# Kernel tuning notes

Hardware: AMD Instinct MI355X
Metric: run time of the kernel (lower is better)

## Reference

```python
import jax, jax.numpy as jnp
import numpy as np

B, K, H = 8, 64, 2048
NH, NKV, HD = 16, 4, 128
CTX = 4096
EPS = 1e-6


def _rope_tables(batch, total_len, head_dim):
    inv_freq = 1.0 / (10000.0 ** (np.arange(0, head_dim, 2, dtype=np.float32) / head_dim))
    pos = np.arange(total_len, dtype=np.float32)
    freqs = np.outer(pos, inv_freq)                      # [S, D/2]
    emb = np.concatenate([freqs, freqs], axis=-1)        # [S, D]
    cos = np.broadcast_to(np.cos(emb), (batch, total_len, head_dim))
    sin = np.broadcast_to(np.sin(emb), (batch, total_len, head_dim))
    return jnp.asarray(cos), jnp.asarray(sin)


def setup_inputs() -> dict:
    key = jax.random.key(0)
    ks = jax.random.split(key, 10)
    s = 0.02
    cos, sin = _rope_tables(B, CTX + K, HD)
    return {
        "hidden_states": jax.random.normal(ks[0], (B, K, H), jnp.float32),
        "ctx_k": jax.random.normal(ks[1], (B, CTX, NKV, HD), jnp.float32),
        "ctx_v": jax.random.normal(ks[2], (B, CTX, NKV, HD), jnp.float32),
        "attn_mask": jnp.zeros((B, 1, K, CTX + K), jnp.float32),
        "cos": cos,
        "sin": sin,
        "wq": jax.random.normal(ks[3], (NH * HD, H), jnp.float32) * s,
        "wk": jax.random.normal(ks[4], (NKV * HD, H), jnp.float32) * s,
        "wv": jax.random.normal(ks[5], (NKV * HD, H), jnp.float32) * s,
        "wo": jax.random.normal(ks[6], (H, NH * HD), jnp.float32) * s,
        "q_norm_w": jnp.ones((HD,), jnp.float32),
        "k_norm_w": jnp.ones((HD,), jnp.float32),
    }


def _rms_norm(x, w):
    var = jnp.mean(jnp.square(x), axis=-1, keepdims=True)
    return x * jax.lax.rsqrt(var + EPS) * w


def _rotate_half(x):
    x1, x2 = jnp.split(x, 2, axis=-1)
    return jnp.concatenate([-x2, x1], axis=-1)


def reference(hidden_states, ctx_k, ctx_v, attn_mask, cos, sin,
              wq, wk, wv, wo, q_norm_w, k_norm_w):
    b, k_len, _ = hidden_states.shape
    ctx_len = ctx_k.shape[1]
    groups = NH // NKV

    # projections -> [B, heads, S, D]
    q = (hidden_states @ wq.T).reshape(b, k_len, NH, HD).transpose(0, 2, 1, 3)
    k_noise = (hidden_states @ wk.T).reshape(b, k_len, NKV, HD).transpose(0, 2, 1, 3)
    v_noise = (hidden_states @ wv.T).reshape(b, k_len, NKV, HD).transpose(0, 2, 1, 3)

    # concat context KV (already per-head projected) with noise KV
    k = jnp.concatenate([ctx_k.transpose(0, 2, 1, 3), k_noise], axis=2)  # [B,NKV,ctx+K,D]
    v = jnp.concatenate([ctx_v.transpose(0, 2, 1, 3), v_noise], axis=2)

    # QK RMSNorm over head_dim
    q = _rms_norm(q, q_norm_w)
    k = _rms_norm(k, k_norm_w)

    # RoPE: q occupies the last K positions, k spans all ctx+K positions
    cos_q = cos[:, ctx_len:, :][:, None, :, :]
    sin_q = sin[:, ctx_len:, :][:, None, :, :]
    cos_k = cos[:, None, :, :]
    sin_k = sin[:, None, :, :]
    q = q * cos_q + _rotate_half(q) * sin_q
    k = k * cos_k + _rotate_half(k) * sin_k

    # GQA expand kv heads -> NH heads
    k = jnp.repeat(k, groups, axis=1)  # [B,NH,ctx+K,D]
    v = jnp.repeat(v, groups, axis=1)

    # scaled dot product attention with float mask
    scale = 1.0 / jnp.sqrt(jnp.float32(HD))
    scores = jnp.einsum("bhqd,bhkd->bhqk", q, k) * scale + attn_mask
    probs = jax.nn.softmax(scores, axis=-1)
    attn = jnp.einsum("bhqk,bhkd->bhqd", probs, v)

    out = attn.transpose(0, 2, 1, 3).reshape(b, k_len, NH * HD)
    return out @ wo.T
```

## Files before the change

kernel.cpp:

```cpp
#include <hip/hip_runtime.h>

#define BB   8
#define KQ   64
#define HDIM 2048
#define NH   16
#define NKV  4
#define HD   128
#define CTX  4096
#define TTOT 4160
#define NTILES 65
#define LOG2E 1.4426950408889634f
#define SCALE 0.08838834764831845f
#define QSCALE (SCALE * LOG2E)
#define MFIX 16.34f

typedef unsigned short u16;
typedef unsigned int   u32;
typedef __attribute__((ext_vector_type(8))) short  s16x8;
typedef __attribute__((ext_vector_type(4))) unsigned short u16x4;
typedef __attribute__((ext_vector_type(4))) float  f32x4;
typedef __bf16 bf16x8 __attribute__((ext_vector_type(8)));

__device__ __forceinline__ u16 f2bf(float f) {
    union { __bf16 h; u16 u; } v; v.h = (__bf16)f; return v.u;
}
__device__ __forceinline__ float bf2f(u16 u) {
    union { float f; u32 u; } v; v.u = ((u32)u) << 16;
    return v.f;
}
__device__ __forceinline__ u32 pack2(float a, float b) {
    return (u32)f2bf(a) | ((u32)f2bf(b) << 16);
}
__device__ __forceinline__ f32x4 mfma16(bf16x8 a, bf16x8 b, f32x4 c) {
    return __builtin_amdgcn_mfma_f32_16x16x32_bf16(a, b, c, 0, 0, 0);
}

__global__ __launch_bounds__(256) void cast_all(
    const float* __restrict__ wq, const float* __restrict__ wk,
    const float* __restrict__ wv, const float* __restrict__ wo,
    const float* __restrict__ hs,
    u16* __restrict__ wqkvb, u16* __restrict__ wob, u16* __restrict__ hsb)
{
    const int i = blockIdx.x * 256 + threadIdx.x;
    const float* src; u16* dst;
    if (i < 524288)       { src = wq + (size_t)i * 8;             dst = wqkvb + (size_t)i * 8; }
    else if (i < 655360)  { src = wk + (size_t)(i - 524288) * 8;  dst = wqkvb + (size_t)i * 8; }
    else if (i < 786432)  { src = wv + (size_t)(i - 655360) * 8;  dst = wqkvb + (size_t)i * 8; }
    else if (i < 1310720) { src = wo + (size_t)(i - 786432) * 8;  dst = wob + (size_t)(i - 786432) * 8; }
    else                  { src = hs + (size_t)(i - 1310720) * 8; dst = hsb + (size_t)(i - 1310720) * 8; }
    float4 a = *(const float4*)src;
    float4 b = *(const float4*)(src + 4);
    s16x8 v;
    v[0]=(short)f2bf(a.x); v[1]=(short)f2bf(a.y); v[2]=(short)f2bf(a.z); v[3]=(short)f2bf(a.w);
    v[4]=(short)f2bf(b.x); v[5]=(short)f2bf(b.y); v[6]=(short)f2bf(b.z); v[7]=(short)f2bf(b.w);
    *(s16x8*)dst = v;
}

__global__ __launch_bounds__(256) void prep_mask(
    const float* __restrict__ mask, u16* __restrict__ maskT)
{
    __shared__ float T[64 * 65];
    const int pt = blockIdx.x % 65, b = blockIdx.x / 65;
    const int p0 = pt * 64;
    {
        const int q = threadIdx.x >> 2, pg = (threadIdx.x & 3) * 16;
        const float* src = mask + ((size_t)b * 64 + q) * TTOT + p0 + pg;
#pragma unroll
        for (int v4 = 0; v4 < 4; ++v4) {
            float4 v = *(const float4*)(src + v4 * 4);
            T[q * 65 + pg + v4 * 4 + 0] = fmaf(v.x, LOG2E, -MFIX);
            T[q * 65 + pg + v4 * 4 + 1] = fmaf(v.y, LOG2E, -MFIX);
            T[q * 65 + pg + v4 * 4 + 2] = fmaf(v.z, LOG2E, -MFIX);
            T[q * 65 + pg + v4 * 4 + 3] = fmaf(v.w, LOG2E, -MFIX);
        }
    }
    __syncthreads();
    {
        const int pos = threadIdx.x >> 2, qg = (threadIdx.x & 3) * 16;
        u16* dst = maskT + ((size_t)b * TTOT + p0 + pos) * 64 + qg;
#pragma unroll
        for (int h8 = 0; h8 < 2; ++h8) {
            s16x8 v;
#pragma unroll
            for (int je = 0; je < 8; ++je)
                v[je] = (short)f2bf(T[(qg + h8 * 8 + je) * 65 + pos]);
            *(s16x8*)(dst + h8 * 8) = v;
        }
    }
}

__device__ __forceinline__ void gemm64_body(
    const u16* __restrict__ Ab, const u16* __restrict__ Bb,
    float* __restrict__ Cb, const int ldc, const int ldk, const int Klen,
    u16* Ash, u16* Bsh)
{
    const int tid = threadIdx.x, lane = tid & 63;
    const int w = tid >> 6, wm = w >> 1, wn = w & 1;
    const int l15 = lane & 15, l4 = lane >> 4;
    const int srow = tid >> 2, scol = (tid & 3) * 16;

    f32x4 acc[2][2];
#pragma unroll
    for (int i = 0; i < 2; ++i)
#pragma unroll
        for (int j = 0; j < 2; ++j) acc[i][j] = (f32x4){0.f, 0.f, 0.f, 0.f};

    const u16* ap = Ab + (size_t)srow * ldk + scol;
    const u16* bp = Bb + (size_t)srow * ldk + scol;
    s16x8 ra0 = *(const s16x8*)ap, ra1 = *(const s16x8*)(ap + 8);
    s16x8 rb0 = *(const s16x8*)bp, rb1 = *(const s16x8*)(bp + 8);
    __builtin_amdgcn_sched_barrier(0);

    for (int k0 = 0; k0 < Klen; k0 += 64) {
        __syncthreads();
        *(s16x8*)(Ash + srow * 72 + scol)     = ra0;
        *(s16x8*)(Ash + srow * 72 + scol + 8) = ra1;
        *(s16x8*)(Bsh + srow * 72 + scol)     = rb0;
        *(s16x8*)(Bsh + srow * 72 + scol + 8) = rb1;
        __syncthreads();
        if (k0 + 64 < Klen) {
            const u16* ap2 = ap + k0 + 64;
            const u16* bp2 = bp + k0 + 64;
            ra0 = *(const s16x8*)ap2; ra1 = *(const s16x8*)(ap2 + 8);
            rb0 = *(const s16x8*)bp2; rb1 = *(const s16x8*)(bp2 + 8);
            __builtin_amdgcn_sched_barrier(0);
        }
#pragma unroll
        for (int ks = 0; ks < 2; ++ks) {
            bf16x8 am[2], bb[2];
#pragma unroll
            for (int i = 0; i < 2; ++i) {
                am[i] = *(const bf16x8*)(Ash + (wm * 32 + i * 16 + l15) * 72 + ks * 32 + l4 * 8);
                bb[i] = *(const bf16x8*)(Bsh + (wn * 32 + i * 16 + l15) * 72 + ks * 32 + l4 * 8);
            }
#pragma unroll
            for (int i = 0; i < 2; ++i)
#pragma unroll
                for (int j = 0; j < 2; ++j)
                    acc[i][j] = mfma16(am[i], bb[j], acc[i][j]);
        }
    }

    float* Cw = Cb + (size_t)(wm * 32) * ldc + wn * 32;
#pragma unroll
    for (int i = 0; i < 2; ++i)
#pragma unroll
        for (int j = 0; j < 2; ++j)
#pragma unroll
            for (int r = 0; r < 4; ++r)
                Cw[(size_t)(i * 16 + l4 * 4 + r) * ldc + j * 16 + l15] = acc[i][j][r];
}

__global__ __launch_bounds__(256) void gemm_qkv_sk(
    const u16* __restrict__ hsb, const u16* __restrict__ wqkvb,
    float* __restrict__ qkvp)
{
    __shared__ __align__(16) u16 Ash[64 * 72];
    __shared__ __align__(16) u16 Bsh[64 * 72];
    const int wid = (blockIdx.x & 7) * 192 + (blockIdx.x >> 3);
    const int y = wid >> 5, rem = wid & 31, kc = rem >> 3, x = rem & 7;
    const int koff = kc * 512;
    const u16* Ab = hsb + (size_t)x * 64 * HDIM + koff;
    const u16* Bb = wqkvb + (size_t)y * 64 * HDIM + koff;
    float* Cb = qkvp + (size_t)kc * 512 * 3072 + (size_t)x * 64 * 3072 + y * 64;
    gemm64_body(Ab, Bb, Cb, 3072, HDIM, 512, Ash, Bsh);
}

__global__ __launch_bounds__(256) void gemm_out_sk(
    const u16* __restrict__ attnb, const u16* __restrict__ wob,
    float* __restrict__ outp)
{
    __shared__ __align__(16) u16 Ash[64 * 72];
    __shared__ __align__(16) u16 Bsh[64 * 72];
    const int wid = (blockIdx.x & 7) * 128 + (blockIdx.x >> 3);
    const int y = wid >> 5, rem = wid & 31, kc = rem >> 3, x = rem & 7;
    const int koff = kc * 512;
    const u16* Ab = attnb + (size_t)x * 64 * HDIM + koff;
    const u16* Bb = wob + (size_t)y * 64 * HDIM + koff;
    float* Cb = outp + (size_t)kc * 512 * 2048 + (size_t)x * 64 * 2048 + y * 64;
    gemm64_body(Ab, Bb, Cb, 2048, HDIM, 512, Ash, Bsh);
}

__global__ __launch_bounds__(256) void reduce4(
    const float* __restrict__ p, float* __restrict__ out, const size_t chunk)
{
    const size_t i = ((size_t)blockIdx.x * 256 + threadIdx.x) * 4;
    float4 a = *(const float4*)(p + i);
    float4 b = *(const float4*)(p + i + chunk);
    float4 c = *(const float4*)(p + i + 2 * chunk);
    float4 d = *(const float4*)(p + i + 3 * chunk);
    float4 r;
    r.x = (a.x + b.x) + (c.x + d.x);
    r.y = (a.y + b.y) + (c.y + d.y);
    r.z = (a.z + b.z) + (c.z + d.z);
    r.w = (a.w + b.w) + (c.w + d.w);
    *(float4*)(out + i) = r;
}

__device__ __forceinline__ void norm_rope_vals(
    float2 xa, float2 xb, const float* __restrict__ wgt,
    const float* __restrict__ cosT, const float* __restrict__ sinT,
    int pos, int j, float outScale, u16* __restrict__ dst)
{
    float ss = xa.x * xa.x + xa.y * xa.y + xb.x * xb.x + xb.y * xb.y;
#pragma unroll
    for (int m = 1; m < 32; m <<= 1) ss += __shfl_xor(ss, m);
    const float rr = rsqrtf(ss * (1.0f / 128.0f) + 1e-6f);
    float2 wa = *(const float2*)(wgt + 2 * j);
    float2 wb = *(const float2*)(wgt + 2 * j + 64);
    float2 ca = *(const float2*)(cosT + (size_t)pos * 128 + 2 * j);
    float2 sa = *(const float2*)(sinT + (size_t)pos * 128 + 2 * j);
    const float nax = xa.x * rr * wa.x, nay = xa.y * rr * wa.y;
    const float nbx = xb.x * rr * wb.x, nby = xb.y * rr * wb.y;
    const float lox = (nax * ca.x - nbx * sa.x) * outScale;
    const float loy = (nay * ca.y - nby * sa.y) * outScale;
    const float hix = (nbx * ca.x + nax * sa.x) * outScale;
    const float hiy = (nby * ca.y + nay * sa.y) * outScale;
    ((u32*)dst)[j]      = pack2(lox, loy);
    ((u32*)dst)[j + 32] = pack2(hix, hiy);
}

__global__ __launch_bounds__(256) void finalize_qkv(
    const float* __restrict__ qkvp, const float* __restrict__ qw,
    const float* __restrict__ kw, const float* __restrict__ cosT,
    const float* __restrict__ sinT,
    u16* __restrict__ Qb, u16* __restrict__ knb, u16* __restrict__ vnb)
{
    const int unit = blockIdx.x * 8 + (threadIdx.x >> 5);
    const int j = threadIdx.x & 31;
    const int slot = unit % 24, bq = unit / 24;
    const int b = bq >> 6, q = bq & 63;
    const int col0 = (slot < 16) ? slot * 128
                   : (slot < 20) ? 2048 + (slot - 16) * 128
                                 : 2560 + (slot - 20) * 128;
    const float* base = qkvp + (size_t)bq * 3072 + col0;

    float2 xa = {0.f, 0.f}, xb = {0.f, 0.f};
#pragma unroll
    for (int kc = 0; kc < 4; ++kc) {
        const float* p = base + (size_t)kc * 512 * 3072;
        float2 a = *(const float2*)(p + 2 * j);
        float2 c = *(const float2*)(p + 2 * j + 64);
        xa.x += a.x; xa.y += a.y; xb.x += c.x; xb.y += c.y;
    }

    if (slot < 16) {
        norm_rope_vals(xa, xb, qw, cosT, sinT, CTX + q, j, QSCALE,
                       Qb + ((size_t)((b * 16 + slot) * 64 + q)) * 128);
    } else if (slot < 20) {
        norm_rope_vals(xa, xb, kw, cosT, sinT, CTX + q, j, 1.0f,
                       knb + ((size_t)((b * 4 + (slot - 16)) * 64 + q)) * 128);
    } else {
        u16* dst = vnb + ((size_t)((b * 4 + (slot - 20)) * 64 + q)) * 128;
        ((u32*)dst)[j]      = pack2(xa.x, xa.y);
        ((u32*)dst)[j + 32] = pack2(xb.x, xb.y);
    }
}

__global__ __launch_bounds__(256) void build_ctx_k(
    const float* __restrict__ ctxk, const float* __restrict__ kw,
    const float* __restrict__ cosT, const float* __restrict__ sinT,
    const u16* __restrict__ knb, u16* __restrict__ Kb)
{
    const int bid = blockIdx.x;
    if (bid < 8192) {
        const int unit = bid * 4 + (threadIdx.x >> 6);
        const int lane = threadIdx.x & 63;
        const int kv = lane >> 4, seg = lane & 15;
        const int b = unit >> 12, pos = unit & 4095;
        const float* src = ctxk + ((size_t)unit * 4 + kv) * 128 + seg * 4;
        float4 xa = *(const float4*)src;
        float4 xb = *(const float4*)(src + 64);
        float ss = xa.x * xa.x + xa.y * xa.y + xa.z * xa.z + xa.w * xa.w
                 + xb.x * xb.x + xb.y * xb.y + xb.z * xb.z + xb.w * xb.w;
        ss += __shfl_xor(ss, 1);
        ss += __shfl_xor(ss, 2);
        ss += __shfl_xor(ss, 4);
        ss += __shfl_xor(ss, 8);
        const float rr = rsqrtf(ss * (1.0f / 128.0f) + 1e-6f);
        float4 ca = *(const float4*)(cosT + (size_t)pos * 128 + seg * 4);
        float4 sa = *(const float4*)(sinT + (size_t)pos * 128 + seg * 4);
        float4 wa = *(const float4*)(kw + seg * 4);
        float4 wb = *(const float4*)(kw + 64 + seg * 4);
        const float nax = xa.x * rr * wa.x, nay = xa.y * rr * wa.y;
        const float naz = xa.z * rr * wa.z, naw = xa.w * rr * wa.w;
        const float nbx = xb.x * rr * wb.x, nby = xb.y * rr * wb.y;
        const float nbz = xb.z * rr * wb.z, nbw = xb.w * rr * wb.w;
        u16x4 vlo, vhi;
        vlo[0] = f2bf(nax * ca.x - nbx * sa.x);
        vlo[1] = f2bf(nay * ca.y - nby * sa.y);
        vlo[2] = f2bf(naz * ca.z - nbz * sa.z);
        vlo[3] = f2bf(naw * ca.w - nbw * sa.w);
        vhi[0] = f2bf(nbx * ca.x + nax * sa.x);
        vhi[1] = f2bf(nby * ca.y + nay * sa.y);
        vhi[2] = f2bf(nbz * ca.z + naz * sa.z);
        vhi[3] = f2bf(nbw * ca.w + naw * sa.w);
        u16* dst = Kb + ((size_t)(b * 4 + kv) * TTOT + pos) * 128 + seg * 4;
        *(u16x4*)dst = vlo;
        *(u16x4*)(dst + 64) = vhi;
    } else {
        const int idx = bid - 8192;
        const u16* src = knb + (size_t)idx * 64 * 128;
        u16* dst = Kb + ((size_t)idx * TTOT + 4096) * 128;
#pragma unroll
        for (int it = 0; it < 4; ++it) {
            const int e = (it * 256 + threadIdx.x) * 8;
            *(s16x8*)(dst + e) = *(const s16x8*)(src + e);
        }
    }
}

__global__ __launch_bounds__(256) void build_ctx_v(
    const float* __restrict__ ctxv, const u16* __restrict__ vnb,
    u16* __restrict__ VtG)
{
    __shared__ __align__(16) float Vt[64 * 130];
    const int bid = blockIdx.x;
    if (bid < 2048) {
        const int pt = bid & 63, kv = (bid >> 6) & 3, b = bid >> 8;
        const int p0 = pt * 64;
        const float* src = ctxv + ((size_t)(b * 4096 + p0) * 4 + kv) * 128;
#pragma unroll
        for (int it = 0; it < 8; ++it) {
            const int g = it * 256 + threadIdx.x;
            const int row = g >> 5, c4 = (g & 31) * 4;
            *(float4*)(&Vt[row * 130 + c4]) = *(const float4*)(src + (size_t)row * 512 + c4);
        }
        __syncthreads();
        const int d = threadIdx.x & 127, half = threadIdx.x >> 7;
        u16* dst = VtG + ((size_t)(b * 4 + kv) * 128 + d) * TTOT + p0 + half * 32;
#pragma unroll
        for (int q8 = 0; q8 < 4; ++q8) {
            s16x8 v;
#pragma unroll
            for (int je = 0; je < 8; ++je)
                v[je] = (short)f2bf(Vt[(half * 32 + q8 * 8 + je) * 130 + d]);
            *(s16x8*)(dst + q8 * 8) = v;
        }
    } else {
        const int idx = bid - 2048;
        const u16* src = vnb + (size_t)idx * 64 * 128;
        u16* dstb = VtG + (size_t)idx * 128 * TTOT + 4096;
        const int d = threadIdx.x & 127, qh = threadIdx.x >> 7;
        u16* dst = dstb + (size_t)d * TTOT + qh * 32;
#pragma unroll
        for (int q8 = 0; q8 < 4; ++q8) {
            s16x8 v;
#pragma unroll
            for (int je = 0; je < 8; ++je)
                v[je] = (short)src[(size_t)(qh * 32 + q8 * 8 + je) * 128 + d];
            *(s16x8*)(dst + q8 * 8) = v;
        }
    }
}

template <int S>
__global__ __launch_bounds__(512, 2) void attn_partial(
    const u16* __restrict__ Qb, const u16* __restrict__ Kb, const u16* __restrict__ VtG,
    const u16* __restrict__ maskT, u16* __restrict__ Opart, float* __restrict__ lsum)
{
    __shared__ __align__(16) u16 Ksh[2][64 * 136];
    __shared__ __align__(16) u16 Vsh[2][128 * 72];
    __shared__ __align__(16) u16 Msh[2][64 * 72];
    __shared__ __align__(16) u16 Psh[8][32 * 40];

    const int s = blockIdx.x, kv = blockIdx.y, b = blockIdx.z;
    const int tid = threadIdx.x, lane = tid & 63, w = tid >> 6;
    const int h = kv * 4 + (w >> 1);
    const int qh = w & 1, qbase = qh * 32;
    const int l15 = lane & 15, l4 = lane >> 4;
    const int t0 = (NTILES * s) / S, t1 = (NTILES * (s + 1)) / S;

    bf16x8 aq[2][4];
    {
        const u16* qb = Qb + ((size_t)((b * 16 + h) * 64 + qbase)) * 128;
#pragma unroll
        for (int mt = 0; mt < 2; ++mt)
#pragma unroll
            for (int ks = 0; ks < 4; ++ks)
                aq[mt][ks] = *(const bf16x8*)(qb + (mt * 16 + l15) * 128 + ks * 32 + l4 * 8);
    }

    bf16x8 bones;
    {
        __bf16 e = (l15 == 0) ? (__bf16)1.0f : (__bf16)0.0f;
#pragma unroll
        for (int i = 0; i < 8; ++i) bones[i] = e;
    }

    f32x4 o[2][8], ol[2];
#pragma unroll
    for (int mt = 0; mt < 2; ++mt) {
        ol[mt] = (f32x4){0.f, 0.f, 0.f, 0.f};
#pragma unroll
        for (int nt = 0; nt < 8; ++nt) o[mt][nt] = (f32x4){0.f, 0.f, 0.f, 0.f};
    }

    const u16* Kbase = Kb + (size_t)(b * 4 + kv) * TTOT * 128;
    const u16* Vbase = VtG + (size_t)(b * 4 + kv) * 128 * TTOT;
    const u16* mrow = maskT + (size_t)b * TTOT * 64;
    u16* P = Psh[w];

    const int kp = tid >> 4, kd8 = (tid & 15) * 8;
    const int vr = tid >> 3, vc8 = (tid & 7) * 8;
    const int mpos = tid >> 3, mq8 = (tid & 7) * 8;

    s16x8 rk0, rk1, rv0, rv1, rm;

    auto ld = [&](int t) {
        const int p = t * 64;
        rk0 = *(const s16x8*)(Kbase + (size_t)(p + kp) * 128 + kd8);
        rk1 = *(const s16x8*)(Kbase + (size_t)(p + kp + 32) * 128 + kd8);
        rv0 = *(const s16x8*)(Vbase + (size_t)vr * TTOT + p + vc8);
        rv1 = *(const s16x8*)(Vbase + (size_t)(vr + 64) * TTOT + p + vc8);
        rm  = *(const s16x8*)(mrow + (size_t)(p + mpos) * 64 + mq8);
        __builtin_amdgcn_sched_barrier(0);
    };
    auto st = [&](int buf) {
        *(s16x8*)(Ksh[buf] + kp * 136 + kd8) = rk0;
        *(s16x8*)(Ksh[buf] + (kp + 32) * 136 + kd8) = rk1;
        *(s16x8*)(Vsh[buf] + vr * 72 + vc8) = rv0;
        *(s16x8*)(Vsh[buf] + (vr + 64) * 72 + vc8) = rv1;
        *(s16x8*)(Msh[buf] + mpos * 72 + mq8) = rm;
    };

    ld(t0);
    st(0);
    __syncthreads();
    if (t0 + 1 < t1) ld(t0 + 1);

    int cur = 0;
    for (int t = t0; t < t1; ++t) {
        f32x4 sc[2][4];
#pragma unroll
        for (int mt = 0; mt < 2; ++mt)
#pragma unroll
            for (int nt = 0; nt < 4; ++nt) sc[mt][nt] = (f32x4){0.f, 0.f, 0.f, 0.f};
        __builtin_amdgcn_s_setprio(1);
#pragma unroll
        for (int nt = 0; nt < 4; ++nt) {
#pragma unroll
            for (int ks = 0; ks < 4; ++ks) {
                bf16x8 bk = *(const bf16x8*)(Ksh[cur] + (nt * 16 + l15) * 136 + ks * 32 + l4 * 8);
                sc[0][nt] = mfma16(aq[0][ks], bk, sc[0][nt]);
                sc[1][nt] = mfma16(aq[1][ks], bk, sc[1][nt]);
            }
        }
        __builtin_amdgcn_s_setprio(0);

#pragma unroll
        for (int mt = 0; mt < 2; ++mt) {
#pragma unroll
            for (int nt = 0; nt < 4; ++nt) {
                u16x4 m4 = *(const u16x4*)(Msh[cur] + (nt * 16 + l15) * 72 + qbase + mt * 16 + l4 * 4);
#pragma unroll
                for (int r = 0; r < 4; ++r)
                    sc[mt][nt][r] = exp2f(sc[mt][nt][r] + bf2f(m4[r]));
            }
        }

#pragma unroll
        for (int ks = 0; ks < 2; ++ks) {
#pragma unroll
            for (int mt = 0; mt < 2; ++mt)
#pragma unroll
                for (int r = 0; r < 4; ++r) {
                    P[(mt * 16 + l4 * 4 + r) * 40 + l15]      = f2bf(sc[mt][ks * 2 + 0][r]);
                    P[(mt * 16 + l4 * 4 + r) * 40 + 16 + l15] = f2bf(sc[mt][ks * 2 + 1][r]);
                }
            bf16x8 ap0 = *(const bf16x8*)(P + (l15) * 40 + l4 * 8);
            bf16x8 ap1 = *(const bf16x8*)(P + (16 + l15) * 40 + l4 * 8);
            __builtin_amdgcn_s_setprio(1);
#pragma unroll
            for (int nt = 0; nt < 8; ++nt) {
                bf16x8 bv = *(const bf16x8*)(Vsh[cur] + (nt * 16 + l15) * 72 + ks * 32 + l4 * 8);
                o[0][nt] = mfma16(ap0, bv, o[0][nt]);
                o[1][nt] = mfma16(ap1, bv, o[1][nt]);
            }
            ol[0] = mfma16(ap0, bones, ol[0]);
            ol[1] = mfma16(ap1, bones, ol[1]);
            __builtin_amdgcn_s_setprio(0);
        }

        if (t + 1 < t1) st(cur ^ 1);
        __syncthreads();
        if (t + 2 < t1) ld(t + 2);
        cur ^= 1;
    }

    {
        u16* ob = Opart + ((size_t)((b * 16 + h) * S + s)) * 8192;
#pragma unroll
        for (int mt = 0; mt < 2; ++mt)
#pragma unroll
            for (int nt = 0; nt < 8; ++nt) {
                u16x4 v;
#pragma unroll
                for (int r = 0; r < 4; ++r) v[r] = f2bf(o[mt][nt][r]);
                *(u16x4*)(ob + (((qh * 2 + mt) * 8 + nt) * 64 + lane) * 4) = v;
            }
        if (l15 == 0) {
#pragma unroll
            for (int mt = 0; mt < 2; ++mt)
#pragma unroll
                for (int r = 0; r < 4; ++r) {
                    const int q = qbase + mt * 16 + l4 * 4 + r;
                    lsum[((size_t)((b * 16 + h) * 64 + q)) * S + s] = ol[mt][r];
                }
        }
    }
}

template <int S>
__global__ __launch_bounds__(256) void merge_kernel(
    const u16* __restrict__ Opart, const float* __restrict__ lsum, u16* __restrict__ attnb)
{
    const int wid = blockIdx.x * 4 + (threadIdx.x >> 6);
    const int lane = threadIdx.x & 63;
    const int l15 = lane & 15, l4 = lane >> 4;
    const int qh = wid & 1, bh = wid >> 1;
    const int h = bh & 15, b = bh >> 4;

    float L = 0.f;
    {
        const float* lr = lsum + ((size_t)bh * 64 + qh * 32 + (lane & 31)) * S;
#pragma unroll
        for (int s2 = 0; s2 < S; ++s2) L += lr[s2];
    }
    const float invL = 1.0f / L;

    float acc[2][8][4];
#pragma unroll
    for (int mt = 0; mt < 2; ++mt)
#pragma unroll
        for (int nt = 0; nt < 8; ++nt)
#pragma unroll
            for (int r = 0; r < 4; ++r) acc[mt][nt][r] = 0.f;

    for (int s2 = 0; s2 < S; ++s2) {
        const u16* ob = Opart + ((size_t)(bh * S + s2)) * 8192;
#pragma unroll
        for (int mt = 0; mt < 2; ++mt)
#pragma unroll
            for (int nt = 0; nt < 8; ++nt) {
                u16x4 v = *(const u16x4*)(ob + (((qh * 2 + mt) * 8 + nt) * 64 + lane) * 4);
#pragma unroll
                for (int r = 0; r < 4; ++r) acc[mt][nt][r] += bf2f(v[r]);
            }
    }

#pragma unroll
    for (int mt = 0; mt < 2; ++mt)
#pragma unroll
        for (int r = 0; r < 4; ++r) {
            const float wl = __shfl(invL, mt * 16 + l4 * 4 + r);
            const int q = qh * 32 + mt * 16 + l4 * 4 + r;
            u16* dst = attnb + (size_t)(b * 64 + q) * 2048 + h * 128;
#pragma unroll
            for (int nt = 0; nt < 8; ++nt)
                dst[nt * 16 + l15] = f2bf(acc[mt][nt][r] * wl);
        }
}

extern "C" void kernel_launch(void* const* d_in, const int* in_sizes, int n_in,
                              void* d_out, int out_size, void* d_ws, size_t ws_size,
                              hipStream_t stream)
{
    (void)in_sizes; (void)n_in; (void)out_size; (void)ws_size;
    const float* hs   = (const float*)d_in[0];
    const float* ctxk = (const float*)d_in[1];
    const float* ctxv = (const float*)d_in[2];
    const float* mask = (const float*)d_in[3];
    const float* cosT = (const float*)d_in[4];
    const float* sinT = (const float*)d_in[5];
    const float* wq   = (const float*)d_in[6];
    const float* wk   = (const float*)d_in[7];
    const float* wv   = (const float*)d_in[8];
    const float* wo   = (const float*)d_in[9];
    const float* qnw  = (const float*)d_in[10];
    const float* knw  = (const float*)d_in[11];

    const int S = 8;

    char* ws = (char*)d_ws;
    size_t off = 0;
    auto carve = [&](size_t bytes) -> void* {
        void* p = ws + off;
        off += (bytes + 255) & ~(size_t)255;
        return p;
    };
    u16*   Qb    = (u16*)carve((size_t)BB * NH * 64 * 128 * 2);
    u16*   Kb    = (u16*)carve((size_t)BB * NKV * TTOT * 128 * 2);
    u16*   VtG   = (u16*)carve((size_t)BB * NKV * TTOT * 128 * 2);
    u16*   Opart = (u16*)carve((size_t)BB * NH * S * 8192 * 2);
    float* lsumb = (float*)carve((size_t)BB * NH * 64 * S * 4);
    u16*   attnb = (u16*)carve((size_t)512 * 2048 * 2);
    u16*   wob   = (u16*)carve((size_t)2048 * 2048 * 2);
    u16*   knb   = (u16*)carve((size_t)BB * NKV * 64 * 128 * 2);
    u16*   vnb   = (u16*)carve((size_t)BB * NKV * 64 * 128 * 2);
    u16*   maskT = (u16*)carve((size_t)BB * TTOT * 64 * 2);
    u16*   wqkvb = (u16*)Kb;
    float* qkvp  = (float*)VtG;
    u16*   hsb   = (u16*)Opart;
    float* outp  = (float*)Kb;

    cast_all<<<5632, 256, 0, stream>>>(wq, wk, wv, wo, hs, wqkvb, wob, hsb);
    prep_mask<<<520, 256, 0, stream>>>(mask, maskT);
    gemm_qkv_sk<<<1536, 256, 0, stream>>>(hsb, wqkvb, qkvp);
    finalize_qkv<<<1536, 256, 0, stream>>>(qkvp, qnw, knw, cosT, sinT, Qb, knb, vnb);
    build_ctx_k<<<8224, 256, 0, stream>>>(ctxk, knw, cosT, sinT, knb, Kb);
    build_ctx_v<<<2080, 256, 0, stream>>>(ctxv, vnb, VtG);
    attn_partial<8><<<dim3(8, NKV, BB), 512, 0, stream>>>(Qb, Kb, VtG, maskT, Opart, lsumb);
    merge_kernel<8><<<64, 256, 0, stream>>>(Opart, lsumb, attnb);
    gemm_out_sk<<<1024, 256, 0, stream>>>(attnb, wob, outp);
    reduce4<<<1024, 256, 0, stream>>>(outp, (float*)d_out, (size_t)512 * 2048);
}
```

Measured before the change: 141.0 us.

## Fuse context-K RMSNorm and RoPE into attention tile loads

Removes the separate build_ctx_k pass that wrote a normalized, rotated bf16 K buffer. The attention kernel now loads raw fp32 context K plus bf16 cos/sin halves and applies RMSNorm and RoPE while staging each tile into shared memory. The noise K rows are read directly from the small knb buffer. This trades a full K write and re-read for doubled fp32 K load width and extra ALU and shuffle work inside the attention loop, and rounds cos/sin to bf16. Buffer aliasing in the workspace is reshuffled to fit the new cos/sin arrays.

```diff
diff --git a/kernel.cpp b/kernel.cpp
--- a/kernel.cpp
+++ b/kernel.cpp
@@ -38,16 +38,22 @@
 __global__ __launch_bounds__(256) void cast_all(
     const float* __restrict__ wq, const float* __restrict__ wk,
     const float* __restrict__ wv, const float* __restrict__ wo,
-    const float* __restrict__ hs,
-    u16* __restrict__ wqkvb, u16* __restrict__ wob, u16* __restrict__ hsb)
+    const float* __restrict__ hs, const float* __restrict__ cosT,
+    const float* __restrict__ sinT,
+    u16* __restrict__ wqkvb, u16* __restrict__ wob, u16* __restrict__ hsb,
+    u16* __restrict__ cosb, u16* __restrict__ sinb)
 {
     const int i = blockIdx.x * 256 + threadIdx.x;
     const float* src; u16* dst;
-    if (i < 524288)       { src = wq + (size_t)i * 8;             dst = wqkvb + (size_t)i * 8; }
-    else if (i < 655360)  { src = wk + (size_t)(i - 524288) * 8;  dst = wqkvb + (size_t)i * 8; }
-    else if (i < 786432)  { src = wv + (size_t)(i - 655360) * 8;  dst = wqkvb + (size_t)i * 8; }
-    else if (i < 1310720) { src = wo + (size_t)(i - 786432) * 8;  dst = wob + (size_t)(i - 786432) * 8; }
-    else                  { src = hs + (size_t)(i - 1310720) * 8; dst = hsb + (size_t)(i - 1310720) * 8; }
+    if (i < 524288)        { src = wq + (size_t)i * 8;             dst = wqkvb + (size_t)i * 8; }
+    else if (i < 655360)   { src = wk + (size_t)(i - 524288) * 8;  dst = wqkvb + (size_t)i * 8; }
+    else if (i < 786432)   { src = wv + (size_t)(i - 655360) * 8;  dst = wqkvb + (size_t)i * 8; }
+    else if (i < 1310720)  { src = wo + (size_t)(i - 786432) * 8;  dst = wob + (size_t)(i - 786432) * 8; }
+    else if (i < 1441792)  { src = hs + (size_t)(i - 1310720) * 8; dst = hsb + (size_t)(i - 1310720) * 8; }
+    else if (i < 1475072)  { const int l = (i - 1441792) * 8;
+                             src = cosT + (size_t)(l >> 6) * 128 + (l & 63); dst = cosb + l; }
+    else                   { const int l = (i - 1475072) * 8;
+                             src = sinT + (size_t)(l >> 6) * 128 + (l & 63); dst = sinb + l; }
     float4 a = *(const float4*)src;
     float4 b = *(const float4*)(src + 4);
     s16x8 v;
@@ -257,59 +263,6 @@
     }
 }
 
-__global__ __launch_bounds__(256) void build_ctx_k(
-    const float* __restrict__ ctxk, const float* __restrict__ kw,
-    const float* __restrict__ cosT, const float* __restrict__ sinT,
-    const u16* __restrict__ knb, u16* __restrict__ Kb)
-{
-    const int bid = blockIdx.x;
-    if (bid < 8192) {
-        const int unit = bid * 4 + (threadIdx.x >> 6);
-        const int lane = threadIdx.x & 63;
-        const int kv = lane >> 4, seg = lane & 15;
-        const int b = unit >> 12, pos = unit & 4095;
-        const float* src = ctxk + ((size_t)unit * 4 + kv) * 128 + seg * 4;
-        float4 xa = *(const float4*)src;
-        float4 xb = *(const float4*)(src + 64);
-        float ss = xa.x * xa.x + xa.y * xa.y + xa.z * xa.z + xa.w * xa.w
-                 + xb.x * xb.x + xb.y * xb.y + xb.z * xb.z + xb.w * xb.w;
-        ss += __shfl_xor(ss, 1);
-        ss += __shfl_xor(ss, 2);
-        ss += __shfl_xor(ss, 4);
-        ss += __shfl_xor(ss, 8);
-        const float rr = rsqrtf(ss * (1.0f / 128.0f) + 1e-6f);
-        float4 ca = *(const float4*)(cosT + (size_t)pos * 128 + seg * 4);
-        float4 sa = *(const float4*)(sinT + (size_t)pos * 128 + seg * 4);
-        float4 wa = *(const float4*)(kw + seg * 4);
-        float4 wb = *(const float4*)(kw + 64 + seg * 4);
-        const float nax = xa.x * rr * wa.x, nay = xa.y * rr * wa.y;
-        const float naz = xa.z * rr * wa.z, naw = xa.w * rr * wa.w;
-        const float nbx = xb.x * rr * wb.x, nby = xb.y * rr * wb.y;
-        const float nbz = xb.z * rr * wb.z, nbw = xb.w * rr * wb.w;
-        u16x4 vlo, vhi;
-        vlo[0] = f2bf(nax * ca.x - nbx * sa.x);
-        vlo[1] = f2bf(nay * ca.y - nby * sa.y);
-        vlo[2] = f2bf(naz * ca.z - nbz * sa.z);
-        vlo[3] = f2bf(naw * ca.w - nbw * sa.w);
-        vhi[0] = f2bf(nbx * ca.x + nax * sa.x);
-        vhi[1] = f2bf(nby * ca.y + nay * sa.y);
-        vhi[2] = f2bf(nbz * ca.z + naz * sa.z);
-        vhi[3] = f2bf(nbw * ca.w + naw * sa.w);
-        u16* dst = Kb + ((size_t)(b * 4 + kv) * TTOT + pos) * 128 + seg * 4;
-        *(u16x4*)dst = vlo;
-        *(u16x4*)(dst + 64) = vhi;
-    } else {
-        const int idx = bid - 8192;
-        const u16* src = knb + (size_t)idx * 64 * 128;
-        u16* dst = Kb + ((size_t)idx * TTOT + 4096) * 128;
-#pragma unroll
-        for (int it = 0; it < 4; ++it) {
-            const int e = (it * 256 + threadIdx.x) * 8;
-            *(s16x8*)(dst + e) = *(const s16x8*)(src + e);
-        }
-    }
-}
-
 __global__ __launch_bounds__(256) void build_ctx_v(
     const float* __restrict__ ctxv, const u16* __restrict__ vnb,
     u16* __restrict__ VtG)
@@ -356,8 +309,11 @@
 
 template <int S>
 __global__ __launch_bounds__(512, 2) void attn_partial(
-    const u16* __restrict__ Qb, const u16* __restrict__ Kb, const u16* __restrict__ VtG,
-    const u16* __restrict__ maskT, u16* __restrict__ Opart, float* __restrict__ lsum)
+    const u16* __restrict__ Qb, const float* __restrict__ ctxk,
+    const float* __restrict__ knw, const u16* __restrict__ cosb,
+    const u16* __restrict__ sinb, const u16* __restrict__ knb,
+    const u16* __restrict__ VtG, const u16* __restrict__ maskT,
+    u16* __restrict__ Opart, float* __restrict__ lsum)
 {
     __shared__ __align__(16) u16 Ksh[2][64 * 136];
     __shared__ __align__(16) u16 Vsh[2][128 * 72];
@@ -371,6 +327,15 @@
     const int l15 = lane & 15, l4 = lane >> 4;
     const int t0 = (NTILES * s) / S, t1 = (NTILES * (s + 1)) / S;
 
+    const int krow = tid >> 3, kg8 = (tid & 7) * 8;
+    const int vr = tid >> 3, vc8 = (tid & 7) * 8;
+    const int mpos = tid >> 3, mq8 = (tid & 7) * 8;
+
+    const float4 w0 = *(const float4*)(knw + kg8);
+    const float4 w1 = *(const float4*)(knw + kg8 + 4);
+    const float4 w2 = *(const float4*)(knw + kg8 + 64);
+    const float4 w3 = *(const float4*)(knw + kg8 + 68);
+
     bf16x8 aq[2][4];
     {
         const u16* qb = Qb + ((size_t)((b * 16 + h) * 64 + qbase)) * 128;
@@ -396,29 +361,69 @@
         for (int nt = 0; nt < 8; ++nt) o[mt][nt] = (f32x4){0.f, 0.f, 0.f, 0.f};
     }
 
-    const u16* Kbase = Kb + (size_t)(b * 4 + kv) * TTOT * 128;
+    const u16* Kn    = knb + (size_t)(b * 4 + kv) * 64 * 128;
     const u16* Vbase = VtG + (size_t)(b * 4 + kv) * 128 * TTOT;
-    const u16* mrow = maskT + (size_t)b * TTOT * 64;
+    const u16* mrow  = maskT + (size_t)b * TTOT * 64;
     u16* P = Psh[w];
 
-    const int kp = tid >> 4, kd8 = (tid & 15) * 8;
-    const int vr = tid >> 3, vc8 = (tid & 7) * 8;
-    const int mpos = tid >> 3, mq8 = (tid & 7) * 8;
-
-    s16x8 rk0, rk1, rv0, rv1, rm;
+    float4 rx0, rx1, rx2, rx3;
+    s16x8 rcs, rsn;
+    s16x8 rkn0, rkn1;
+    s16x8 rv0, rv1, rm;
+    int tin = -1;
 
     auto ld = [&](int t) {
         const int p = t * 64;
-        rk0 = *(const s16x8*)(Kbase + (size_t)(p + kp) * 128 + kd8);
-        rk1 = *(const s16x8*)(Kbase + (size_t)(p + kp + 32) * 128 + kd8);
+        if (t < 64) {
+            const float* kp_ = ctxk + (((size_t)(b * 4096 + p + krow)) * 4 + kv) * 128 + kg8;
+            rx0 = *(const float4*)kp_;        rx1 = *(const float4*)(kp_ + 4);
+            rx2 = *(const float4*)(kp_ + 64); rx3 = *(const float4*)(kp_ + 68);
+            rcs = *(const s16x8*)(cosb + (size_t)(p + krow) * 64 + kg8);
+            rsn = *(const s16x8*)(sinb + (size_t)(p + krow) * 64 + kg8);
+        } else {
+            const u16* kp2 = Kn + (size_t)krow * 128 + kg8;
+            rkn0 = *(const s16x8*)kp2;
+            rkn1 = *(const s16x8*)(kp2 + 64);
+        }
         rv0 = *(const s16x8*)(Vbase + (size_t)vr * TTOT + p + vc8);
         rv1 = *(const s16x8*)(Vbase + (size_t)(vr + 64) * TTOT + p + vc8);
         rm  = *(const s16x8*)(mrow + (size_t)(p + mpos) * 64 + mq8);
+        tin = t;
         __builtin_amdgcn_sched_barrier(0);
     };
     auto st = [&](int buf) {
-        *(s16x8*)(Ksh[buf] + kp * 136 + kd8) = rk0;
-        *(s16x8*)(Ksh[buf] + (kp + 32) * 136 + kd8) = rk1;
+        if (tin < 64) {
+            float ss = rx0.x*rx0.x + rx0.y*rx0.y + rx0.z*rx0.z + rx0.w*rx0.w
+                     + rx1.x*rx1.x + rx1.y*rx1.y + rx1.z*rx1.z + rx1.w*rx1.w
+                     + rx2.x*rx2.x + rx2.y*rx2.y + rx2.z*rx2.z + rx2.w*rx2.w
+                     + rx3.x*rx3.x + rx3.y*rx3.y + rx3.z*rx3.z + rx3.w*rx3.w;
+            ss += __shfl_xor(ss, 1);
+            ss += __shfl_xor(ss, 2);
+            ss += __shfl_xor(ss, 4);
+            const float rr = rsqrtf(ss * (1.0f / 128.0f) + 1e-6f);
+            s16x8 klo, khi;
+#define KROPE(i, xl, xh, wl, wh)                                     \
+            {                                                        \
+                const float nlo = xl * rr * wl, nhi = xh * rr * wh;  \
+                const float c = bf2f((u16)rcs[i]), sn = bf2f((u16)rsn[i]); \
+                klo[i] = (short)f2bf(nlo * c - nhi * sn);            \
+                khi[i] = (short)f2bf(nhi * c + nlo * sn);            \
+            }
+            KROPE(0, rx0.x, rx2.x, w0.x, w2.x)
+            KROPE(1, rx0.y, rx2.y, w0.y, w2.y)
+            KROPE(2, rx0.z, rx2.z, w0.z, w2.z)
+            KROPE(3, rx0.w, rx2.w, w0.w, w2.w)
+            KROPE(4, rx1.x, rx3.x, w1.x, w3.x)
+            KROPE(5, rx1.y, rx3.y, w1.y, w3.y)
+            KROPE(6, rx1.z, rx3.z, w1.z, w3.z)
+            KROPE(7, rx1.w, rx3.w, w1.w, w3.w)
+#undef KROPE
+            *(s16x8*)(Ksh[buf] + krow * 136 + kg8)      = klo;
+            *(s16x8*)(Ksh[buf] + krow * 136 + 64 + kg8) = khi;
+        } else {
+            *(s16x8*)(Ksh[buf] + krow * 136 + kg8)      = rkn0;
+            *(s16x8*)(Ksh[buf] + krow * 136 + 64 + kg8) = rkn1;
+        }
         *(s16x8*)(Vsh[buf] + vr * 72 + vc8) = rv0;
         *(s16x8*)(Vsh[buf] + (vr + 64) * 72 + vc8) = rv1;
         *(s16x8*)(Msh[buf] + mpos * 72 + mq8) = rm;
@@ -590,27 +595,29 @@
         return p;
     };
     u16*   Qb    = (u16*)carve((size_t)BB * NH * 64 * 128 * 2);
-    u16*   Kb    = (u16*)carve((size_t)BB * NKV * TTOT * 128 * 2);
     u16*   VtG   = (u16*)carve((size_t)BB * NKV * TTOT * 128 * 2);
     u16*   Opart = (u16*)carve((size_t)BB * NH * S * 8192 * 2);
     float* lsumb = (float*)carve((size_t)BB * NH * 64 * S * 4);
     u16*   attnb = (u16*)carve((size_t)512 * 2048 * 2);
     u16*   wob   = (u16*)carve((size_t)2048 * 2048 * 2);
+    u16*   wqkvb = (u16*)carve((size_t)3072 * 2048 * 2);
     u16*   knb   = (u16*)carve((size_t)BB * NKV * 64 * 128 * 2);
     u16*   vnb   = (u16*)carve((size_t)BB * NKV * 64 * 128 * 2);
     u16*   maskT = (u16*)carve((size_t)BB * TTOT * 64 * 2);
-    u16*   wqkvb = (u16*)Kb;
-    float* qkvp  = (float*)VtG;
-    u16*   hsb   = (u16*)Opart;
-    float* outp  = (float*)Kb;
-
-    cast_all<<<5632, 256, 0, stream>>>(wq, wk, wv, wo, hs, wqkvb, wob, hsb);
+    u16*   cosb  = (u16*)carve((size_t)TTOT * 64 * 2);
+    u16*   sinb  = (u16*)carve((size_t)TTOT * 64 * 2);
+    float* qkvp = (float*)VtG;
+    u16*   hsb  = (u16*)Opart;
+    float* outp = (float*)Opart;
+
+    cast_all<<<5892, 256, 0, stream>>>(wq, wk, wv, wo, hs, cosT, sinT,
+                                       wqkvb, wob, hsb, cosb, sinb);
     prep_mask<<<520, 256, 0, stream>>>(mask, maskT);
     gemm_qkv_sk<<<1536, 256, 0, stream>>>(hsb, wqkvb, qkvp);
     finalize_qkv<<<1536, 256, 0, stream>>>(qkvp, qnw, knw, cosT, sinT, Qb, knb, vnb);
-    build_ctx_k<<<8224, 256, 0, stream>>>(ctxk, knw, cosT, sinT, knb, Kb);
     build_ctx_v<<<2080, 256, 0, stream>>>(ctxv, vnb, VtG);
-    attn_partial<8><<<dim3(8, NKV, BB), 512, 0, stream>>>(Qb, Kb, VtG, maskT, Opart, lsumb);
+    attn_partial<8><<<dim3(8, NKV, BB), 512, 0, stream>>>(
+        Qb, ctxk, knw, cosb, sinb, knb, VtG, maskT, Opart, lsumb);
     merge_kernel<8><<<64, 256, 0, stream>>>(Opart, lsumb, attnb);
     gemm_out_sk<<<1024, 256, 0, stream>>>(attnb, wob, outp);
     reduce4<<<1024, 256, 0, stream>>>(outp, (float*)d_out, (size_t)512 * 2048);
```

After: 133.1 us. 5.6% less time.
